# Kernel optimization log

Hardware: AMD Instinct MI355X
Metric: run time of the kernel (lower is better)

## Reference

```python
import jax, jax.numpy as jnp
import numpy as np

B, T, I, H, O, L = 64, 512, 512, 1024, 512, 2


def setup_inputs() -> dict:
    key = jax.random.key(0)
    ks = jax.random.split(key, 12)
    s = 1.0 / np.sqrt(H)
    inp = {
        "source": jax.random.normal(ks[0], (B, T, I), jnp.float32),
        "target": jax.random.normal(ks[1], (B, T, O), jnp.float32),
        # layer 0 GRU params (PyTorch layout: [3H, in], gate order r,z,n)
        "W_ih0": jax.random.uniform(ks[2], (3 * H, I), jnp.float32, -s, s),
        "W_hh0": jax.random.uniform(ks[3], (3 * H, H), jnp.float32, -s, s),
        "b_ih0": jax.random.uniform(ks[4], (3 * H,), jnp.float32, -s, s),
        "b_hh0": jax.random.uniform(ks[5], (3 * H,), jnp.float32, -s, s),
        # layer 1 GRU params
        "W_ih1": jax.random.uniform(ks[6], (3 * H, H), jnp.float32, -s, s),
        "W_hh1": jax.random.uniform(ks[7], (3 * H, H), jnp.float32, -s, s),
        "b_ih1": jax.random.uniform(ks[8], (3 * H,), jnp.float32, -s, s),
        "b_hh1": jax.random.uniform(ks[9], (3 * H,), jnp.float32, -s, s),
        # output projection
        "W_out": jax.random.uniform(ks[10], (O, H), jnp.float32, -s, s),
        "b_out": jax.random.uniform(ks[11], (O,), jnp.float32, -s, s),
    }
    return inp


def _gru_cell(x, h, W_ih, W_hh, b_ih, b_hh):
    # x: [B, in], h: [B, H]; PyTorch GRU gate order (r, z, n)
    gi = x @ W_ih.T + b_ih   # [B, 3H]
    gh = h @ W_hh.T + b_hh   # [B, 3H]
    ir, iz, inn = jnp.split(gi, 3, axis=-1)
    hr, hz, hn = jnp.split(gh, 3, axis=-1)
    r = jax.nn.sigmoid(ir + hr)
    z = jax.nn.sigmoid(iz + hz)
    n = jnp.tanh(inn + r * hn)
    return (1.0 - z) * n + z * h


def reference(source, target, W_ih0, W_hh0, b_ih0, b_hh0,
              W_ih1, W_hh1, b_ih1, b_hh1, W_out, b_out):
    xs = jnp.swapaxes(source, 0, 1)  # [T, B, I]
    h0 = jnp.zeros((source.shape[0], H), source.dtype)

    def step(carry, x_t):
        h_l0, h_l1 = carry
        h_l0 = _gru_cell(x_t, h_l0, W_ih0, W_hh0, b_ih0, b_hh0)
        h_l1 = _gru_cell(h_l0, h_l1, W_ih1, W_hh1, b_ih1, b_hh1)
        out_t = h_l1 @ W_out.T + b_out  # [B, O]
        return (h_l0, h_l1), out_t

    _, outputs = jax.lax.scan(step, (h0, h0), xs)
    return outputs  # [T, B, O], matching the original seq-first outputs buffer
```

## Files before the change

kernel.cpp:

```cpp
#include <hip/hip_runtime.h>
#include <hip/hip_fp16.h>
#include <cmath>

#define BDIM 64
#define TLEN 512
#define IDIM 512
#define HDIM 1024
#define ODIM 512
#define NBLK 256
#define NTHR 512
#define PF 8

typedef _Float16 h16;
typedef _Float16 half8 __attribute__((ext_vector_type(8)));
typedef float f32x4 __attribute__((ext_vector_type(4)));

__device__ __forceinline__ float sigf(float x){ return 1.f/(1.f+__expf(-x)); }

#define PLANE_ELEMS (2*2*4*32*64*8)
__device__ __forceinline__ size_t poff(int slot,int pl,int bt,int k8){
    return ((((size_t)slot*2+pl)*4+bt)*32 + (size_t)k8)*512;
}

__device__ __forceinline__ void st_b128_sc1(void* p, f32x4 v){
    asm volatile("global_store_dwordx4 %0, %1, off sc1" :: "v"(p), "v"(v) : "memory");
}

__global__ void gru_init(h16* __restrict__ planes, int* __restrict__ ctrl){
    size_t n = 2*(size_t)PLANE_ELEMS;
    for (size_t i = (size_t)blockIdx.x*blockDim.x + threadIdx.x; i < n;
         i += (size_t)gridDim.x*blockDim.x)
        planes[i] = (h16)0.f;
    if (blockIdx.x==0 && threadIdx.x<256) ctrl[threadIdx.x] = 0;
}

__global__ __launch_bounds__(NTHR,1)
void gru_persist(const float* __restrict__ src,
                 const float* __restrict__ Wih0, const float* __restrict__ Whh0,
                 const float* __restrict__ bih0, const float* __restrict__ bhh0,
                 const float* __restrict__ Wih1, const float* __restrict__ Whh1,
                 const float* __restrict__ bih1, const float* __restrict__ bhh1,
                 const float* __restrict__ Wout, const float* __restrict__ bout,
                 float* __restrict__ out,
                 h16* __restrict__ h0pl, h16* __restrict__ h1pl,
                 int* __restrict__ ctrl)
{
    extern __shared__ char lds[];
    const int tid  = threadIdx.x;
    const int lane = tid & 63;
    const int wv   = __builtin_amdgcn_readfirstlane(tid >> 6);
    const int bt   = wv & 3;
    const int kh2  = wv >> 2;
    const int bk   = blockIdx.x;
    const int role = (bk >= 128);
    const int ib   = role ? bk - 128 : bk;
    const int U    = 8 * ib;
    const int K8   = role ? 64 : 48;

    h16*   Alds = (h16*)lds;
    float* scr  = (float*)(lds + (size_t)2*K8*64*8*sizeof(h16));
    h16*   hstg = (h16*)(lds + (size_t)2*K8*64*8*sizeof(h16) + 16384);

    {
        const int t = tid >> 8;
        const int m = (tid >> 4) & 15;
        for (int k8 = (tid & 15); k8 < K8; k8 += 16) {
            for (int q = 0; q < 4; ++q) {
                half8 hv;
                #pragma unroll
                for (int j = 0; j < 8; ++j) {
                    const int c = k8*32 + q*8 + j;
                    float v;
                    if (!role) {
                        if (t == 1 && m >= 8) v = 0.f;
                        else {
                            int grow = (t==0) ? ((m<8)? U+m : HDIM+U+(m-8)) : (2*HDIM+U+m);
                            v = (c < IDIM) ? Wih0[(size_t)grow*IDIM + c]
                                           : Whh0[(size_t)grow*HDIM + (c-IDIM)];
                        }
                    } else {
                        if (t == 1 && m >= 8) {
                            if (m < 12) {
                                int o = 4*ib + (m-8);
                                v = (c < HDIM) ? 0.f : Wout[(size_t)o*HDIM + (c-HDIM)];
                            } else v = 0.f;
                        } else {
                            int grow = (t==0) ? ((m<8)? U+m : HDIM+U+(m-8)) : (2*HDIM+U+m);
                            v = (c < HDIM) ? Wih1[(size_t)grow*HDIM + c]
                                           : Whh1[(size_t)grow*HDIM + (c-HDIM)];
                        }
                    }
                    hv[j] = (h16)v;
                }
                *(half8*)&Alds[(((size_t)t*K8 + k8)*64 + q*16 + m)*8] = hv;
            }
        }
    }

    const int eu = tid >> 6, eb = tid & 63;
    float br,bz,bnx,bnh;
    if (!role){ br = bih0[U+eu]+bhh0[U+eu]; bz = bih0[HDIM+U+eu]+bhh0[HDIM+U+eu];
                bnx = bih0[2*HDIM+U+eu];    bnh = bhh0[2*HDIM+U+eu]; }
    else      { br = bih1[U+eu]+bhh1[U+eu]; bz = bih1[HDIM+U+eu]+bhh1[HDIM+U+eu];
                bnx = bih1[2*HDIM+U+eu];    bnh = bhh1[2*HDIM+U+eu]; }
    float bo = 0.f;
    if (role && tid < 256) bo = bout[4*ib + (tid>>6)];
    float hprev = 0.f;

    __syncthreads();

    auto barrier = [&](int p){
        asm volatile("s_waitcnt vmcnt(0)" ::: "memory");
        __syncthreads();
        if (wv == 0) {
            const int tgt = p + 1;
            if (lane == 0)
                __hip_atomic_store(&ctrl[bk], tgt, __ATOMIC_RELAXED, __HIP_MEMORY_SCOPE_AGENT);
            for (;;) {
                int a = __hip_atomic_load(&ctrl[lane      ], __ATOMIC_RELAXED, __HIP_MEMORY_SCOPE_AGENT);
                int b = __hip_atomic_load(&ctrl[lane +  64], __ATOMIC_RELAXED, __HIP_MEMORY_SCOPE_AGENT);
                int c = __hip_atomic_load(&ctrl[lane + 128], __ATOMIC_RELAXED, __HIP_MEMORY_SCOPE_AGENT);
                int d = __hip_atomic_load(&ctrl[lane + 192], __ATOMIC_RELAXED, __HIP_MEMORY_SCOPE_AGENT);
                if (__all((a>=tgt)&&(b>=tgt)&&(c>=tgt)&&(d>=tgt))) break;
                __builtin_amdgcn_s_sleep(2);
            }
            __builtin_amdgcn_fence(__ATOMIC_ACQUIRE, "agent");
            asm volatile("s_waitcnt vmcnt(0)" ::: "memory");
        }
        __syncthreads();
    };

    for (int p = 0; p <= TLEN+1; ++p) {
        const bool act = role ? (p >= 1) : (p < TLEN);
        if (act) {
            f32x4 acc00 = {0.f,0.f,0.f,0.f}, acc01 = {0.f,0.f,0.f,0.f};
            f32x4 acc10 = {0.f,0.f,0.f,0.f}, acc11 = {0.f,0.f,0.f,0.f};

            auto planeLoop = [&](int lo, int hi, int koff2,
                                 const h16* BHp, const h16* BLp,
                                 f32x4& aX0, f32x4& aX1){
                half8 bufH[PF], bufL[PF];
                #pragma unroll
                for (int i = 0; i < PF; ++i) {
                    size_t o = ((size_t)(lo + i - koff2)*64 + lane)*8;
                    bufH[i] = *(const half8*)(BHp + o);
                    bufL[i] = *(const half8*)(BLp + o);
                }
                for (int base = lo; base < hi; base += PF) {
                    #pragma unroll
                    for (int i = 0; i < PF; ++i) {
                        const int k8 = base + i;
                        half8 bh = bufH[i], bl = bufL[i];
                        if (k8 + PF < hi) {
                            size_t o = ((size_t)(k8 + PF - koff2)*64 + lane)*8;
                            bufH[i] = *(const half8*)(BHp + o);
                            bufL[i] = *(const half8*)(BLp + o);
                        }
                        half8 a0 = *(const half8*)&Alds[(((size_t)0*K8 + k8)*64 + lane)*8];
                        half8 a1 = *(const half8*)&Alds[(((size_t)1*K8 + k8)*64 + lane)*8];
                        aX0 = __builtin_amdgcn_mfma_f32_16x16x32_f16(a0, bh, aX0, 0,0,0);
                        aX0 = __builtin_amdgcn_mfma_f32_16x16x32_f16(a0, bl, aX0, 0,0,0);
                        aX1 = __builtin_amdgcn_mfma_f32_16x16x32_f16(a1, bh, aX1, 0,0,0);
                        aX1 = __builtin_amdgcn_mfma_f32_16x16x32_f16(a1, bl, aX1, 0,0,0);
                    }
                }
            };
            auto srcLoop = [&](f32x4& aX0, f32x4& aX1){
                const float* xb = src + ((size_t)(bt*16 + (lane&15))*TLEN + p)*IDIM
                                      + (lane>>4)*8;
                float4 f0[PF], f1[PF];
                #pragma unroll
                for (int i = 0; i < PF; ++i) {
                    f0[i] = *(const float4*)(xb + i*32);
                    f1[i] = *(const float4*)(xb + i*32 + 4);
                }
                for (int base = 0; base < 16; base += PF) {
                    #pragma unroll
                    for (int i = 0; i < PF; ++i) {
                        const int k8 = base + i;
                        float ff[8] = {f0[i].x,f0[i].y,f0[i].z,f0[i].w,
                                       f1[i].x,f1[i].y,f1[i].z,f1[i].w};
                        half8 bh, bl;
                        #pragma unroll
                        for (int j = 0; j < 8; ++j) {
                            h16 hv = (h16)ff[j];
                            bh[j] = hv; bl[j] = (h16)(ff[j] - (float)hv);
                        }
                        if (k8 + PF < 16) {
                            f0[i] = *(const float4*)(xb + (k8+PF)*32);
                            f1[i] = *(const float4*)(xb + (k8+PF)*32 + 4);
                        }
                        half8 a0 = *(const half8*)&Alds[(((size_t)0*K8 + k8)*64 + lane)*8];
                        half8 a1 = *(const half8*)&Alds[(((size_t)1*K8 + k8)*64 + lane)*8];
                        aX0 = __builtin_amdgcn_mfma_f32_16x16x32_f16(a0, bh, aX0, 0,0,0);
                        aX0 = __builtin_amdgcn_mfma_f32_16x16x32_f16(a0, bl, aX0, 0,0,0);
                        aX1 = __builtin_amdgcn_mfma_f32_16x16x32_f16(a1, bh, aX1, 0,0,0);
                        aX1 = __builtin_amdgcn_mfma_f32_16x16x32_f16(a1, bl, aX1, 0,0,0);
                    }
                }
            };

            if (!role) {
                const h16* BH = h0pl + poff((p-1)&1,0,bt,0);
                const h16* BL = BH + 65536;
                if (kh2 == 0) { srcLoop(acc00, acc10); planeLoop(16,24,16,BH,BL,acc01,acc11); }
                else          { planeLoop(24,48,16,BH,BL,acc01,acc11); }
            } else {
                if (kh2 == 0) { const h16* BH = h0pl + poff((p-1)&1,0,bt,0);
                                planeLoop(0,32,0,BH,BH+65536,acc00,acc10); }
                else          { const h16* BH = h1pl + poff( p   &1,0,bt,0);
                                planeLoop(32,64,32,BH,BH+65536,acc01,acc11); }
            }

            if (kh2 == 1) {
                #pragma unroll
                for (int r = 0; r < 4; ++r) {
                    scr[(((bt*2+0)*2+0)*4+r)*64 + lane] = acc00[r];
                    scr[(((bt*2+0)*2+1)*4+r)*64 + lane] = acc01[r];
                    scr[(((bt*2+1)*2+0)*4+r)*64 + lane] = acc10[r];
                    scr[(((bt*2+1)*2+1)*4+r)*64 + lane] = acc11[r];
                }
            }
            __syncthreads();
            if (kh2 == 0) {
                #pragma unroll
                for (int r = 0; r < 4; ++r) {
                    scr[(((bt*2+0)*2+0)*4+r)*64 + lane] += acc00[r];
                    scr[(((bt*2+0)*2+1)*4+r)*64 + lane] += acc01[r];
                    scr[(((bt*2+1)*2+0)*4+r)*64 + lane] += acc10[r];
                    scr[(((bt*2+1)*2+1)*4+r)*64 + lane] += acc11[r];
                }
            }
            __syncthreads();

            const bool doh = (!role || p <= TLEN);
            {
                const int bte = eb>>4, le = eb&15, lq = eu>>2, rr = eu&3;
                auto rdv = [&](int t,int ab,int q)->float{
                    return scr[(((bte*2+t)*2+ab)*4+rr)*64 + q*16 + le];
                };
                float rv = rdv(0,0,lq)   + rdv(0,1,lq)   + br;
                float zv = rdv(0,0,2+lq) + rdv(0,1,2+lq) + bz;
                float nx = rdv(1,0,lq) + bnx;
                float nh = rdv(1,1,lq) + bnh;
                float r = sigf(rv), z = sigf(zv);
                float n = tanhf(nx + r*nh);
                float h = (1.f - z)*n + z*hprev;
                if (doh) {
                    hprev = h;
                    h16 hh = (h16)h;
                    h16 hl = (h16)(h - (float)hh);
                    hstg[((0*4 + (eb>>4))*16 + (eb&15))*8 + eu] = hh;
                    hstg[((1*4 + (eb>>4))*16 + (eb&15))*8 + eu] = hl;
                }
            }
            if (role && p >= 2 && tid < 256) {
                const int ro = tid >> 6, b = tid & 63;
                float v = scr[((((b>>4)*2+1)*2+1)*4 + ro)*64 + 32 + (b&15)] + bo;
                out[((size_t)(p-2)*BDIM + b)*ODIM + (4*ib + ro)] = v;
            }
            __syncthreads();
            if (doh && tid < 128) {
                const int pl = tid >> 6, bts = (tid >> 4) & 3, le = tid & 15;
                const int slot = (!role) ? (p&1) : ((p-1)&1);
                h16* basep = (!role) ? h0pl : h1pl;
                size_t g = poff(slot, pl, bts, U>>5) + (size_t)(((U>>3)&3)*16 + le)*8;
                f32x4 v = *(f32x4*)&hstg[(((size_t)pl*4 + bts)*16 + le)*8];
                st_b128_sc1(basep + g, v);
            }
        }
        barrier(p);
    }
}

extern "C" void kernel_launch(void* const* d_in, const int* in_sizes, int n_in,
                              void* d_out, int out_size, void* d_ws, size_t ws_size,
                              hipStream_t stream)
{
    const float* src  = (const float*)d_in[0];
    const float* Wih0 = (const float*)d_in[2];
    const float* Whh0 = (const float*)d_in[3];
    const float* bih0 = (const float*)d_in[4];
    const float* bhh0 = (const float*)d_in[5];
    const float* Wih1 = (const float*)d_in[6];
    const float* Whh1 = (const float*)d_in[7];
    const float* bih1 = (const float*)d_in[8];
    const float* bhh1 = (const float*)d_in[9];
    const float* Wout = (const float*)d_in[10];
    const float* bout = (const float*)d_in[11];
    float* out = (float*)d_out;

    h16* h0pl = (h16*)d_ws;
    h16* h1pl = h0pl + PLANE_ELEMS;
    int* ctrl = (int*)((char*)d_ws + 2*(size_t)PLANE_ELEMS*sizeof(h16));

    const int ldsBytes = 2*64*64*8*2 + 4*2*2*4*64*4 + 2*4*16*8*2;
    (void)hipFuncSetAttribute((const void*)gru_persist,
                              hipFuncAttributeMaxDynamicSharedMemorySize, ldsBytes);

    hipLaunchKernelGGL(gru_init, dim3(256), dim3(256), 0, stream, h0pl, ctrl);
    hipLaunchKernelGGL(gru_persist, dim3(NBLK), dim3(NTHR), ldsBytes, stream,
                       src, Wih0, Whh0, bih0, bhh0, Wih1, Whh1, bih1, bhh1,
                       Wout, bout, out, h0pl, h1pl, ctrl);
}
```

Before: 8.358 ms.

## Replace acquire fence with sc1 inline-asm loads and explicit vmcnt pipelining

Drops the agent-scope acquire fence after the grid barrier. The hidden-state plane reads are switched to inline-asm global_load_dwordx4 with sc1 so they bypass stale cache without a full invalidate. The prefetch ring now uses explicit s_waitcnt vmcnt counters and a peeled tail, so MFMAs wait only on the loads they need. This relies on sc1 loads giving coherence in place of the fence. Hand-managed vmcnt counting is fragile if the compiler issues other memory ops in between.

```diff
diff --git a/kernel.cpp b/kernel.cpp
--- a/kernel.cpp
+++ b/kernel.cpp
@@ -24,6 +24,18 @@
 
 __device__ __forceinline__ void st_b128_sc1(void* p, f32x4 v){
     asm volatile("global_store_dwordx4 %0, %1, off sc1" :: "v"(p), "v"(v) : "memory");
+}
+
+__device__ __forceinline__ void wait_vm(int n){
+    if      (n<=0)  asm volatile("s_waitcnt vmcnt(0)");
+    else if (n==2)  asm volatile("s_waitcnt vmcnt(2)");
+    else if (n==4)  asm volatile("s_waitcnt vmcnt(4)");
+    else if (n==6)  asm volatile("s_waitcnt vmcnt(6)");
+    else if (n==8)  asm volatile("s_waitcnt vmcnt(8)");
+    else if (n==10) asm volatile("s_waitcnt vmcnt(10)");
+    else if (n==12) asm volatile("s_waitcnt vmcnt(12)");
+    else            asm volatile("s_waitcnt vmcnt(14)");
+    __builtin_amdgcn_sched_barrier(0);
 }
 
 __global__ void gru_init(h16* __restrict__ planes, int* __restrict__ ctrl){
@@ -124,8 +136,6 @@
                 if (__all((a>=tgt)&&(b>=tgt)&&(c>=tgt)&&(d>=tgt))) break;
                 __builtin_amdgcn_s_sleep(2);
             }
-            __builtin_amdgcn_fence(__ATOMIC_ACQUIRE, "agent");
-            asm volatile("s_waitcnt vmcnt(0)" ::: "memory");
         }
         __syncthreads();
     };
@@ -137,32 +147,47 @@
             f32x4 acc10 = {0.f,0.f,0.f,0.f}, acc11 = {0.f,0.f,0.f,0.f};
 
             auto planeLoop = [&](int lo, int hi, int koff2,
-                                 const h16* BHp, const h16* BLp,
+                                 const half8* BHp, const half8* BLp,
                                  f32x4& aX0, f32x4& aX1){
                 half8 bufH[PF], bufL[PF];
+                asm volatile("s_waitcnt vmcnt(0)" ::: "memory");
                 #pragma unroll
                 for (int i = 0; i < PF; ++i) {
-                    size_t o = ((size_t)(lo + i - koff2)*64 + lane)*8;
-                    bufH[i] = *(const half8*)(BHp + o);
-                    bufL[i] = *(const half8*)(BLp + o);
-                }
-                for (int base = lo; base < hi; base += PF) {
+                    size_t o = (size_t)(lo + i - koff2)*64 + lane;
+                    asm volatile("global_load_dwordx4 %0, %1, off sc1"
+                                 : "=v"(bufH[i]) : "v"(BHp + o));
+                    asm volatile("global_load_dwordx4 %0, %1, off sc1"
+                                 : "=v"(bufL[i]) : "v"(BLp + o));
+                }
+                int base;
+                for (base = lo; base + PF < hi; base += PF) {
                     #pragma unroll
                     for (int i = 0; i < PF; ++i) {
                         const int k8 = base + i;
-                        half8 bh = bufH[i], bl = bufL[i];
-                        if (k8 + PF < hi) {
-                            size_t o = ((size_t)(k8 + PF - koff2)*64 + lane)*8;
-                            bufH[i] = *(const half8*)(BHp + o);
-                            bufL[i] = *(const half8*)(BLp + o);
-                        }
+                        wait_vm(2*PF-2);
                         half8 a0 = *(const half8*)&Alds[(((size_t)0*K8 + k8)*64 + lane)*8];
                         half8 a1 = *(const half8*)&Alds[(((size_t)1*K8 + k8)*64 + lane)*8];
-                        aX0 = __builtin_amdgcn_mfma_f32_16x16x32_f16(a0, bh, aX0, 0,0,0);
-                        aX0 = __builtin_amdgcn_mfma_f32_16x16x32_f16(a0, bl, aX0, 0,0,0);
-                        aX1 = __builtin_amdgcn_mfma_f32_16x16x32_f16(a1, bh, aX1, 0,0,0);
-                        aX1 = __builtin_amdgcn_mfma_f32_16x16x32_f16(a1, bl, aX1, 0,0,0);
+                        aX0 = __builtin_amdgcn_mfma_f32_16x16x32_f16(a0, bufH[i], aX0, 0,0,0);
+                        aX0 = __builtin_amdgcn_mfma_f32_16x16x32_f16(a0, bufL[i], aX0, 0,0,0);
+                        aX1 = __builtin_amdgcn_mfma_f32_16x16x32_f16(a1, bufH[i], aX1, 0,0,0);
+                        aX1 = __builtin_amdgcn_mfma_f32_16x16x32_f16(a1, bufL[i], aX1, 0,0,0);
+                        size_t o = (size_t)(k8 + PF - koff2)*64 + lane;
+                        asm volatile("global_load_dwordx4 %0, %1, off sc1"
+                                     : "=v"(bufH[i]) : "v"(BHp + o));
+                        asm volatile("global_load_dwordx4 %0, %1, off sc1"
+                                     : "=v"(bufL[i]) : "v"(BLp + o));
                     }
+                }
+                #pragma unroll
+                for (int i = 0; i < PF; ++i) {
+                    const int k8 = base + i;
+                    wait_vm(2*(PF-1-i));
+                    half8 a0 = *(const half8*)&Alds[(((size_t)0*K8 + k8)*64 + lane)*8];
+                    half8 a1 = *(const half8*)&Alds[(((size_t)1*K8 + k8)*64 + lane)*8];
+                    aX0 = __builtin_amdgcn_mfma_f32_16x16x32_f16(a0, bufH[i], aX0, 0,0,0);
+                    aX0 = __builtin_amdgcn_mfma_f32_16x16x32_f16(a0, bufL[i], aX0, 0,0,0);
+                    aX1 = __builtin_amdgcn_mfma_f32_16x16x32_f16(a1, bufH[i], aX1, 0,0,0);
+                    aX1 = __builtin_amdgcn_mfma_f32_16x16x32_f16(a1, bufL[i], aX1, 0,0,0);
                 }
             };
             auto srcLoop = [&](f32x4& aX0, f32x4& aX1){
@@ -201,15 +226,15 @@
             };
 
             if (!role) {
-                const h16* BH = h0pl + poff((p-1)&1,0,bt,0);
-                const h16* BL = BH + 65536;
+                const half8* BH = (const half8*)(h0pl + poff((p-1)&1,0,bt,0));
+                const half8* BL = BH + 8192;
                 if (kh2 == 0) { srcLoop(acc00, acc10); planeLoop(16,24,16,BH,BL,acc01,acc11); }
                 else          { planeLoop(24,48,16,BH,BL,acc01,acc11); }
             } else {
-                if (kh2 == 0) { const h16* BH = h0pl + poff((p-1)&1,0,bt,0);
-                                planeLoop(0,32,0,BH,BH+65536,acc00,acc10); }
-                else          { const h16* BH = h1pl + poff( p   &1,0,bt,0);
-                                planeLoop(32,64,32,BH,BH+65536,acc01,acc11); }
+                if (kh2 == 0) { const half8* BH = (const half8*)(h0pl + poff((p-1)&1,0,bt,0));
+                                planeLoop(0,32,0,BH,BH+8192,acc00,acc10); }
+                else          { const half8* BH = (const half8*)(h1pl + poff( p   &1,0,bt,0));
+                                planeLoop(32,64,32,BH,BH+8192,acc01,acc11); }
             }
 
             if (kh2 == 1) {
```

Result: faster. 7.033 ms (-15.8%).
